# Kernel optimization log

Measured on AMD Instinct MI355X. Metric: run time of the kernel, lower is better.

## Reference

```python
import jax, jax.numpy as jnp
import numpy as np

MARGIN = 0.2
LAMBDA_SOFTMAX = 9.0
LAMBDA_LSE = 6.0
WEIGHT_FACTOR = 0.7  # attn_prev is absent/zero on the i2t path
EPS = 1e-8
NEG_INF = -1e9


def setup_inputs() -> dict:
    key = jax.random.key(0)
    k1, k2, k3 = jax.random.split(key, 3)
    B, R, W, D = 128, 36, 32, 256  # batch, regions, max words, feat dim
    im = jax.random.normal(k1, (B, R, D), jnp.float32)
    s = jax.random.normal(k2, (B, W, D), jnp.float32)
    s_l = jax.random.randint(k3, (B,), 1, W + 1)  # caption lengths in [1, W]
    return {"im": im, "s": s, "s_l": s_l}


def _xattn_scores_i2t(im, s, s_l):
    # im: (B, R, D) images; s: (C, W, D) captions; s_l: (C,) lengths
    C, W = s.shape[0], s.shape[1]
    word_mask = jnp.arange(W)[None, :] < s_l[:, None]  # (C, W)

    # func_attention(query=images, context=caption words):
    # attn[c,b,w,r] = <s[c,w], im[b,r]>
    attn = jnp.einsum('cwd,brd->cbwr', s, im)
    # raw_feature_norm == 'clipped_l2norm': LeakyReLU(0.1) then l2norm over region axis
    attn = jax.nn.leaky_relu(attn, 0.1)
    attn = attn / (jnp.sqrt(jnp.sum(attn * attn, axis=-1, keepdims=True)) + EPS)
    # softmax over sourceL = words, with smoothing; mask padded words
    logits = jnp.where(word_mask[:, None, :, None], attn * LAMBDA_SOFTMAX, NEG_INF)
    A = jax.nn.softmax(logits, axis=2)  # (C, B, W, R), sums to 1 over words
    # weightedContext[c,b,r,:] = 0.7 * sum_w A[c,b,w,r] * s[c,w,:]
    wC = WEIGHT_FACTOR * jnp.einsum('cbwr,cwd->cbrd', A, s)

    # cosine similarity between image regions and weighted caption context
    num = jnp.sum(im[None] * wC, axis=-1)                      # (C, B, R)
    denom = jnp.linalg.norm(im, axis=-1)[None] * jnp.linalg.norm(wC, axis=-1)
    row_sim = num / jnp.clip(denom, EPS)

    # agg_func == 'LogSumExp' over regions
    sim = jax.nn.logsumexp(LAMBDA_LSE * row_sim, axis=2) / LAMBDA_LSE  # (C, B)
    return sim.T  # scores: (n_image, n_caption)


def reference(im, s, s_l):
    scores = _xattn_scores_i2t(im, s, s_l)
    diag = jnp.diag(scores)
    cost_s = jnp.clip(MARGIN + scores - diag[:, None], 0.0)   # caption retrieval
    cost_im = jnp.clip(MARGIN + scores - diag[None, :], 0.0)  # image retrieval
    eye = jnp.eye(scores.shape[0], dtype=bool)
    cost_s = jnp.where(eye, 0.0, cost_s)
    cost_im = jnp.where(eye, 0.0, cost_im)
    # max_violation=True: hardest negatives
    return jnp.sum(jnp.max(cost_s, axis=1)) + jnp.sum(jnp.max(cost_im, axis=0))
```

## Files before the change

kernel.cpp:

```cpp
#include <hip/hip_runtime.h>
#include <math.h>

#define CN 128
#define RN 36
#define WN 32
#define DN 256

#define SSTR  264
#define GSTR  40
#define ATSTR 40

#define WS_SCORES 0
#define WS_S_SW   65536
#define WS_IM_SW  (WS_S_SW + CN*16384)
#define WS_N2I    (WS_IM_SW + CN*18432)
#define WS_NEED   (WS_N2I + CN*RN*4)

typedef unsigned short u16;
typedef __attribute__((ext_vector_type(4))) unsigned short u16x4;
typedef __attribute__((ext_vector_type(8))) unsigned short u16x8;
typedef __attribute__((ext_vector_type(8))) __bf16 bf16x8;
typedef __attribute__((ext_vector_type(4))) float f32x4;

#define C9   12.9842502f
#define C6   8.65616798f
#define IC6  0.115524530f

__device__ __forceinline__ float bf2f(u16 u){ return __uint_as_float(((unsigned)u)<<16); }
__device__ __forceinline__ u16 f2bf(float f){ unsigned x=__float_as_uint(f); return (u16)((x + 0x7fffu + ((x>>16)&1u))>>16); }
__device__ __forceinline__ u16 f2bf_hw(float f){ __bf16 h = (__bf16)f; return __builtin_bit_cast(u16, h); }
__device__ __forceinline__ float lrelu(float v){ return fmaxf(v, 0.1f*v); }

__device__ __forceinline__ void gload16(const void* g, void* l){
    __builtin_amdgcn_global_load_lds((const __attribute__((address_space(1))) void*)g,
                                     (__attribute__((address_space(3))) void*)l, 16, 0, 0);
}

__global__ __launch_bounds__(256)
void precompute_kernel(const float* __restrict__ im, const float* __restrict__ s,
                       char* __restrict__ ws)
{
    const int tid = threadIdx.x;
    if (blockIdx.x < 128) {
        const int i = blockIdx.x;
        const float* src = s + (size_t)i*(WN*DN);
        u16* out = (u16*)(ws + WS_S_SW) + (size_t)i*8192;
#pragma unroll
        for (int it = 0; it < 4; it++) {
            int idx = tid + it*256;
            int r = idx >> 5, x = idx & 31;
            int jl = (x & 24) | ((x & 7) ^ (r & 7));
            const float4* p = (const float4*)(src + r*DN + jl*8);
            float4 v0 = p[0], v1 = p[1];
            u16x8 hh = { f2bf_hw(v0.x),f2bf_hw(v0.y),f2bf_hw(v0.z),f2bf_hw(v0.w),
                         f2bf_hw(v1.x),f2bf_hw(v1.y),f2bf_hw(v1.z),f2bf_hw(v1.w) };
            *(u16x8*)(out + r*256 + x*8) = hh;
        }
    } else {
        const int i = blockIdx.x - 128;
        const float* src = im + (size_t)i*(RN*DN);
#pragma unroll
        for (int it = 0; it < 5; it++) {
            int idx = tid + it*256;
            if (idx < 1152) {
                int q = idx / 288, rem = idx - q*288;
                int r = rem >> 3, x = rem & 7;
                int jl = x ^ (r & 7);
                const float4* p = (const float4*)(src + r*DN + q*64 + jl*8);
                float4 v0 = p[0], v1 = p[1];
                u16x8 hh = { f2bf_hw(v0.x),f2bf_hw(v0.y),f2bf_hw(v0.z),f2bf_hw(v0.w),
                             f2bf_hw(v1.x),f2bf_hw(v1.y),f2bf_hw(v1.z),f2bf_hw(v1.w) };
                *(u16x8*)(ws + WS_IM_SW + (size_t)q*589824 + (size_t)i*4608 + r*128 + x*16) = hh;
            }
        }
        float* n2o = (float*)(ws + WS_N2I) + (size_t)i*RN;
#pragma unroll
        for (int it = 0; it < 2; it++) {
            int idx = tid + it*256;
            if (idx < 288) {
                int r = idx >> 3, q = idx & 7;
                const float4* p = (const float4*)(src + r*DN + q*32);
                float ss = 0.f;
#pragma unroll
                for (int k = 0; k < 8; k++) {
                    float4 v = p[k];
                    ss = fmaf(v.x,v.x,ss); ss = fmaf(v.y,v.y,ss);
                    ss = fmaf(v.z,v.z,ss); ss = fmaf(v.w,v.w,ss);
                }
                ss += __shfl_xor(ss,1); ss += __shfl_xor(ss,2); ss += __shfl_xor(ss,4);
                if (q == 0) n2o[r] = ss;
            }
        }
    }
}

__global__ __launch_bounds__(512, 2)
void xattn_staged(const int* __restrict__ s_l, char* __restrict__ ws)
{
    __shared__ __align__(16) u16 smem[37376];
    u16* lds_s  = smem;
    u16* lds_im = smem + 16384;
    u16* lds_g  = smem + 34816;
    char* smem_b = (char*)smem;

    const int tid = threadIdx.x;
    const int lane = tid & 63, wv = tid >> 6;
    const int bq = blockIdx.x, cp = blockIdx.y;
    const int ci = wv >> 2, bi = wv & 3;
    const int c = cp*2 + ci, b = bq*4 + bi;
    const int col = lane & 15, g4 = lane >> 4;
    const int gm = bi >> 1, gn = bi & 1;
    const int L = s_l[c];
    const int r2c = (32+col > 35) ? 35 : 32+col;

    const char* ssrc = ws + WS_S_SW + (size_t)(cp*2)*16384;
    const char* ibase = ws + WS_IM_SW + (size_t)(bq*4)*4608;

    auto stage_im = [&](int q, int buf){
        const char* isrc = ibase + (size_t)q*589824;
        char* dbase = smem_b + 32768 + buf*18432;
#pragma unroll
        for (int t = 0; t < 3; t++) {
            int blk = wv + t*8;
            if (blk < 18) gload16(isrc + blk*1024 + lane*16, dbase + blk*1024);
        }
    };

#pragma unroll
    for (int t = 0; t < 7; t++) {
        int blk = wv + t*8;
        if (blk < 50) {
            const char* src; char* dst;
            if (blk < 32) { src = ssrc + blk*1024;         dst = smem_b + blk*1024; }
            else          { src = ibase + (blk-32)*1024;   dst = smem_b + 32768 + (blk-32)*1024; }
            gload16(src + lane*16, dst);
        }
    }

    const float* n2p = (const float*)(ws + WS_N2I) + (size_t)b*RN;
    float n2v0 = n2p[col];
    float n2v1 = n2p[16+col];
    float n2v2 = n2p[r2c];

    f32x4 raw[2][3];
#pragma unroll
    for (int m = 0; m < 2; m++)
#pragma unroll
        for (int n = 0; n < 3; n++) raw[m][n] = (f32x4){0.f,0.f,0.f,0.f};
    f32x4 gacc = {0.f,0.f,0.f,0.f};

    const u16* sbb = lds_s + ci*8192;

    auto computeq = [&](int q, int buf){
        const u16* ibb = lds_im + buf*9216 + bi*2304;
#pragma unroll
        for (int ks = 0; ks < 2; ks++) {
            int chq = ks*4 + g4;
            int swA = chq ^ (col & 7);
            int oA  = (q*8 + swA) * 8;
            int oB  = swA * 8;
            int oB2 = (chq ^ (r2c & 7)) * 8;
            bf16x8 a0 = *(const bf16x8*)&sbb[col*256 + oA];
            bf16x8 a1 = *(const bf16x8*)&sbb[(16+col)*256 + oA];
            bf16x8 ga = *(const bf16x8*)&sbb[(gm*16+col)*256 + oA];
            bf16x8 gb = *(const bf16x8*)&sbb[(gn*16+col)*256 + oA];
            bf16x8 b0 = *(const bf16x8*)&ibb[col*64 + oB];
            bf16x8 b1 = *(const bf16x8*)&ibb[(16+col)*64 + oB];
            bf16x8 b2 = *(const bf16x8*)&ibb[r2c*64 + oB2];
            raw[0][0] = __builtin_amdgcn_mfma_f32_16x16x32_bf16(a0, b0, raw[0][0], 0,0,0);
            raw[0][1] = __builtin_amdgcn_mfma_f32_16x16x32_bf16(a0, b1, raw[0][1], 0,0,0);
            raw[0][2] = __builtin_amdgcn_mfma_f32_16x16x32_bf16(a0, b2, raw[0][2], 0,0,0);
            raw[1][0] = __builtin_amdgcn_mfma_f32_16x16x32_bf16(a1, b0, raw[1][0], 0,0,0);
            raw[1][1] = __builtin_amdgcn_mfma_f32_16x16x32_bf16(a1, b1, raw[1][1], 0,0,0);
            raw[1][2] = __builtin_amdgcn_mfma_f32_16x16x32_bf16(a1, b2, raw[1][2], 0,0,0);
            gacc      = __builtin_amdgcn_mfma_f32_16x16x32_bf16(ga, gb, gacc, 0,0,0);
        }
    };

    __syncthreads();
    stage_im(1, 1); computeq(0, 0);
    __syncthreads();
    stage_im(2, 0); computeq(1, 1);
    __syncthreads();
    stage_im(3, 1); computeq(2, 0);
    __syncthreads();
    computeq(3, 1);

    {
        u16x4 hg = { f2bf_hw(gacc[0]), f2bf_hw(gacc[1]), f2bf_hw(gacc[2]), f2bf_hw(gacc[3]) };
        *(u16x4*)&lds_g[ci*1280 + (gn*16+col)*GSTR + gm*16 + g4*4] = hg;
    }

    float af[2][3][4];
#pragma unroll
    for (int m = 0; m < 2; m++) {
#pragma unroll
        for (int reg = 0; reg < 4; reg++) {
            float ssum = 0.f;
#pragma unroll
            for (int n = 0; n < 3; n++) {
                float v = lrelu(raw[m][n][reg]);
                if (n == 2 && col >= 4) v = 0.f;
                af[m][n][reg] = v;
                ssum = fmaf(v, v, ssum);
            }
            ssum += __shfl_xor(ssum, 1);
            ssum += __shfl_xor(ssum, 2);
            ssum += __shfl_xor(ssum, 4);
            ssum += __shfl_xor(ssum, 8);
            float inv2 = C9 / (sqrtf(ssum) + 1e-8f);
#pragma unroll
            for (int n = 0; n < 3; n++) af[m][n][reg] *= inv2;
        }
    }

    float num[3];
#pragma unroll
    for (int n = 0; n < 3; n++) {
        float nm = 0.f;
#pragma unroll
        for (int m = 0; m < 2; m++)
#pragma unroll
            for (int reg = 0; reg < 4; reg++) {
                int w = m*16 + g4*4 + reg;
                float e = (w < L) ? __builtin_amdgcn_exp2f(af[m][n][reg]) : 0.f;
                af[m][n][reg] = e;
                nm = fmaf(e, raw[m][n][reg], nm);
            }
        nm += __shfl_xor(nm, 16);
        nm += __shfl_xor(nm, 32);
        num[n] = nm;
    }

    __syncthreads();

    u16* at = (u16*)(smem_b + 32768) + wv*1920;
#pragma unroll
    for (int m = 0; m < 2; m++)
#pragma unroll
        for (int n = 0; n < 3; n++) {
            u16x4 h = { f2bf_hw(af[m][n][0]), f2bf_hw(af[m][n][1]),
                        f2bf_hw(af[m][n][2]), f2bf_hw(af[m][n][3]) };
            *(u16x4*)&at[(n*16 + col)*ATSTR + m*16 + g4*4] = h;
        }

    bf16x8 gf0 = *(const bf16x8*)&lds_g[ci*1280 + col*GSTR + g4*8];
    bf16x8 gf1 = *(const bf16x8*)&lds_g[ci*1280 + (16+col)*GSTR + g4*8];

    float qv[3];
#pragma unroll
    for (int n = 0; n < 3; n++) {
        bf16x8 bfv = *(const bf16x8*)&at[(n*16 + col)*ATSTR + g4*8];
        f32x4 z = {0.f,0.f,0.f,0.f};
        f32x4 t0 = __builtin_amdgcn_mfma_f32_16x16x32_bf16(gf0, bfv, z, 0,0,0);
        f32x4 t1 = __builtin_amdgcn_mfma_f32_16x16x32_bf16(gf1, bfv, z, 0,0,0);
        float q = 0.f;
#pragma unroll
        for (int reg = 0; reg < 4; reg++) {
            q = fmaf(af[0][n][reg], t0[reg], q);
            q = fmaf(af[1][n][reg], t1[reg], q);
        }
        q += __shfl_xor(q, 16);
        q += __shfl_xor(q, 32);
        qv[n] = q;
    }

    float rs[3];
    {
        float n2a[3] = { n2v0, n2v1, n2v2 };
#pragma unroll
        for (int n = 0; n < 3; n++) {
            float denom = fmaxf(0.7f * sqrtf(n2a[n] * qv[n]), 1e-8f);
            rs[n] = 0.7f * num[n] / denom;
        }
    }
    float xm = -1e30f;
#pragma unroll
    for (int n = 0; n < 3; n++) {
        bool valid = (n < 2) || (col < 4);
        if (valid) xm = fmaxf(xm, C6 * rs[n]);
    }
    xm = fmaxf(xm, __shfl_xor(xm, 1));
    xm = fmaxf(xm, __shfl_xor(xm, 2));
    xm = fmaxf(xm, __shfl_xor(xm, 4));
    xm = fmaxf(xm, __shfl_xor(xm, 8));
    float es = 0.f;
#pragma unroll
    for (int n = 0; n < 3; n++) {
        bool valid = (n < 2) || (col < 4);
        if (valid) es += __builtin_amdgcn_exp2f(C6 * rs[n] - xm);
    }
    es += __shfl_xor(es, 1);
    es += __shfl_xor(es, 2);
    es += __shfl_xor(es, 4);
    es += __shfl_xor(es, 8);

    if (lane == 0)
        ((float*)(ws + WS_SCORES))[(size_t)b * CN + c] =
            (xm + __builtin_amdgcn_logf(es)) * IC6;
}

__global__ __launch_bounds__(512, 2)
void xattn_fallback(const float* __restrict__ im, const float* __restrict__ s,
                    const int* __restrict__ s_l, float* __restrict__ scores)
{
    __shared__ u16   s_lds[2][WN*SSTR];
    __shared__ u16   im_lds[4][RN*SSTR];
    __shared__ u16   g_lds[2][WN*GSTR];
    __shared__ u16   at_lds[8][48*ATSTR];
    __shared__ float n2i_lds[4][RN];

    const int tid  = threadIdx.x;
    const int lane = tid & 63;
    const int wv   = tid >> 6;
    const int bq   = blockIdx.x, cp = blockIdx.y;
    const int ci   = wv >> 2, bi = wv & 3;
    const int c    = cp*2 + ci, b = bq*4 + bi;
    const int col  = lane & 15, g4 = lane >> 4;

    if (wv < 4) {
        const float4* g = (const float4*)(im + (size_t)(bq*4 + wv) * (RN*DN));
        u16* dst = im_lds[wv];
#pragma unroll
        for (int k = 0; k < 36; k++) {
            int i = lane + k*64;
            float4 v = g[i];
            int row = i >> 6, cc = (i & 63) * 4;
            u16x4 h = { f2bf(v.x), f2bf(v.y), f2bf(v.z), f2bf(v.w) };
            *(u16x4*)&dst[row*SSTR + cc] = h;
        }
    } else {
        int cap = (wv - 4) >> 1;
        int l2  = ((wv - 4) & 1) * 64 + lane;
        const float4* g = (const float4*)(s + (size_t)(cp*2 + cap) * (WN*DN));
        u16* dst = s_lds[cap];
#pragma unroll
        for (int k = 0; k < 16; k++) {
            int i = l2 + k*128;
            float4 v = g[i];
            int row = i >> 6, cc = (i & 63) * 4;
            u16x4 h = { f2bf(v.x), f2bf(v.y), f2bf(v.z), f2bf(v.w) };
            *(u16x4*)&dst[row*SSTR + cc] = h;
        }
    }
    __syncthreads();

    {
        const int gm = (wv >> 1) & 1, gn = wv & 1;
        const u16* sb = s_lds[ci];
        f32x4 acc = {0.f, 0.f, 0.f, 0.f};
#pragma unroll
        for (int ks = 0; ks < 8; ks++) {
            int k0 = ks*32 + g4*8;
            bf16x8 af = *(const bf16x8*)&sb[(gm*16 + col)*SSTR + k0];
            bf16x8 bfv = *(const bf16x8*)&sb[(gn*16 + col)*SSTR + k0];
            acc = __builtin_amdgcn_mfma_f32_16x16x32_bf16(af, bfv, acc, 0, 0, 0);
        }
        u16x4 h = { f2bf(acc[0]), f2bf(acc[1]), f2bf(acc[2]), f2bf(acc[3]) };
        *(u16x4*)&g_lds[ci][(gn*16 + col)*GSTR + gm*16 + g4*4] = h;
    }

    if (wv < 4) {
        const u16* ib = im_lds[wv];
        int r = lane >> 1, half = lane & 1;
        float ss = 0.f;
        const u16x8* p = (const u16x8*)&ib[r*SSTR + half*128];
#pragma unroll
        for (int k = 0; k < 16; k++) {
            u16x8 v = p[k];
#pragma unroll
            for (int j = 0; j < 8; j++) { float f = bf2f(v[j]); ss = fmaf(f, f, ss); }
        }
        ss += __shfl_xor(ss, 1);
        if (half == 0) n2i_lds[wv][r] = ss;
        if (lane < 8) {
            int r2 = 32 + (lane >> 1), h2 = lane & 1;
            float s2 = 0.f;
            const u16x8* p2 = (const u16x8*)&ib[r2*SSTR + h2*128];
#pragma unroll
            for (int k = 0; k < 16; k++) {
                u16x8 v = p2[k];
#pragma unroll
                for (int j = 0; j < 8; j++) { float f = bf2f(v[j]); s2 = fmaf(f, f, s2); }
            }
            s2 += __shfl_xor(s2, 1);
            if (h2 == 0) n2i_lds[wv][r2] = s2;
        }
    }

    const u16* sb = s_lds[ci];
    const u16* ib = im_lds[bi];
    f32x4 raw[2][3];
#pragma unroll
    for (int m = 0; m < 2; m++)
#pragma unroll
        for (int n = 0; n < 3; n++) raw[m][n] = (f32x4){0.f,0.f,0.f,0.f};
    {
        int r2c = 32 + col; if (r2c > 35) r2c = 35;
#pragma unroll
        for (int ks = 0; ks < 8; ks++) {
            int k0 = ks*32 + g4*8;
            bf16x8 a0 = *(const bf16x8*)&sb[col*SSTR + k0];
            bf16x8 a1 = *(const bf16x8*)&sb[(16 + col)*SSTR + k0];
            bf16x8 b0 = *(const bf16x8*)&ib[col*SSTR + k0];
            bf16x8 b1 = *(const bf16x8*)&ib[(16 + col)*SSTR + k0];
            bf16x8 b2 = *(const bf16x8*)&ib[r2c*SSTR + k0];
            raw[0][0] = __builtin_amdgcn_mfma_f32_16x16x32_bf16(a0, b0, raw[0][0], 0,0,0);
            raw[0][1] = __builtin_amdgcn_mfma_f32_16x16x32_bf16(a0, b1, raw[0][1], 0,0,0);
            raw[0][2] = __builtin_amdgcn_mfma_f32_16x16x32_bf16(a0, b2, raw[0][2], 0,0,0);
            raw[1][0] = __builtin_amdgcn_mfma_f32_16x16x32_bf16(a1, b0, raw[1][0], 0,0,0);
            raw[1][1] = __builtin_amdgcn_mfma_f32_16x16x32_bf16(a1, b1, raw[1][1], 0,0,0);
            raw[1][2] = __builtin_amdgcn_mfma_f32_16x16x32_bf16(a1, b2, raw[1][2], 0,0,0);
        }
    }

    float af[2][3][4];
#pragma unroll
    for (int m = 0; m < 2; m++) {
#pragma unroll
        for (int reg = 0; reg < 4; reg++) {
            float ssum = 0.f;
#pragma unroll
            for (int n = 0; n < 3; n++) {
                float v = lrelu(raw[m][n][reg]);
                if (n == 2 && col >= 4) v = 0.f;
                af[m][n][reg] = v;
                ssum = fmaf(v, v, ssum);
            }
            ssum += __shfl_xor(ssum, 1);
            ssum += __shfl_xor(ssum, 2);
            ssum += __shfl_xor(ssum, 4);
            ssum += __shfl_xor(ssum, 8);
            float inv = 1.0f / (sqrtf(ssum) + 1e-8f);
#pragma unroll
            for (int n = 0; n < 3; n++) af[m][n][reg] *= inv;
        }
    }

    const int L = s_l[c];
    float num[3], qv[3];
#pragma unroll
    for (int n = 0; n < 3; n++) {
        float mx = -1e30f;
#pragma unroll
        for (int m = 0; m < 2; m++)
#pragma unroll
            for (int reg = 0; reg < 4; reg++) {
                int w = m*16 + g4*4 + reg;
                if (w < L) mx = fmaxf(mx, af[m][n][reg]);
            }
        mx = fmaxf(mx, __shfl_xor(mx, 16));
        mx = fmaxf(mx, __shfl_xor(mx, 32));
        mx *= 9.0f;
        float sme = 0.f;
#pragma unroll
        for (int m = 0; m < 2; m++)
#pragma unroll
            for (int reg = 0; reg < 4; reg++) {
                int w = m*16 + g4*4 + reg;
                float e = (w < L) ? __expf(fmaf(9.0f, af[m][n][reg], -mx)) : 0.f;
                af[m][n][reg] = e;
                sme += e;
            }
        sme += __shfl_xor(sme, 16);
        sme += __shfl_xor(sme, 32);
        float inv = 1.0f / sme;
        float nm = 0.f;
#pragma unroll
        for (int m = 0; m < 2; m++)
#pragma unroll
            for (int reg = 0; reg < 4; reg++) {
                af[m][n][reg] *= inv;
                nm = fmaf(af[m][n][reg], raw[m][n][reg], nm);
            }
        nm += __shfl_xor(nm, 16);
        nm += __shfl_xor(nm, 32);
        num[n] = nm;
    }

#pragma unroll
    for (int m = 0; m < 2; m++)
#pragma unroll
        for (int n = 0; n < 3; n++) {
            u16x4 h = { f2bf(af[m][n][0]), f2bf(af[m][n][1]),
                        f2bf(af[m][n][2]), f2bf(af[m][n][3]) };
            *(u16x4*)&at_lds[wv][(n*16 + col)*ATSTR + m*16 + g4*4] = h;
        }

    __syncthreads();

    bf16x8 gf0 = *(const bf16x8*)&g_lds[ci][col*GSTR + g4*8];
    bf16x8 gf1 = *(const bf16x8*)&g_lds[ci][(16+col)*GSTR + g4*8];
    f32x4 tt[2][3];
#pragma unroll
    for (int n = 0; n < 3; n++) {
        bf16x8 bfv = *(const bf16x8*)&at_lds[wv][(n*16 + col)*ATSTR + g4*8];
        f32x4 z = {0.f,0.f,0.f,0.f};
        tt[0][n] = __builtin_amdgcn_mfma_f32_16x16x32_bf16(gf0, bfv, z, 0,0,0);
        tt[1][n] = __builtin_amdgcn_mfma_f32_16x16x32_bf16(gf1, bfv, z, 0,0,0);
    }

#pragma unroll
    for (int n = 0; n < 3; n++) {
        float q = 0.f;
#pragma unroll
        for (int m = 0; m < 2; m++)
#pragma unroll
            for (int reg = 0; reg < 4; reg++) q = fmaf(af[m][n][reg], tt[m][n][reg], q);
        q += __shfl_xor(q, 16);
        q += __shfl_xor(q, 32);
        qv[n] = q;
    }

    float rs[3];
#pragma unroll
    for (int n = 0; n < 3; n++) {
        int r = n*16 + col; if (r > 35) r = 35;
        float n2 = n2i_lds[bi][r];
        float denom = fmaxf(0.7f * sqrtf(n2 * qv[n]), 1e-8f);
        rs[n] = 0.7f * num[n] / denom;
    }
    float xm = -1e30f;
#pragma unroll
    for (int n = 0; n < 3; n++) {
        bool valid = (n < 2) || (col < 4);
        if (valid) xm = fmaxf(xm, 6.0f * rs[n]);
    }
    xm = fmaxf(xm, __shfl_xor(xm, 1));
    xm = fmaxf(xm, __shfl_xor(xm, 2));
    xm = fmaxf(xm, __shfl_xor(xm, 4));
    xm = fmaxf(xm, __shfl_xor(xm, 8));
    float es = 0.f;
#pragma unroll
    for (int n = 0; n < 3; n++) {
        bool valid = (n < 2) || (col < 4);
        if (valid) es += __expf(6.0f * rs[n] - xm);
    }
    es += __shfl_xor(es, 1);
    es += __shfl_xor(es, 2);
    es += __shfl_xor(es, 4);
    es += __shfl_xor(es, 8);

    if (lane == 0) scores[(size_t)b * CN + c] = (xm + __logf(es)) / 6.0f;
}

__global__ __launch_bounds__(1024)
void contrastive_loss_kernel(const float* __restrict__ scores,
                             unsigned int* __restrict__ out)
{
    __shared__ float sc[128][129];
    __shared__ float dg[128];
    __shared__ float red[128];
    const int tid = threadIdx.x;

    const float4* s4 = (const float4*)scores;
#pragma unroll
    for (int it = 0; it < 4; it++) {
        int i = tid + it*1024;
        float4 v = s4[i];
        int row = i >> 5, c4 = (i & 31) << 2;
        sc[row][c4+0] = v.x; sc[row][c4+1] = v.y;
        sc[row][c4+2] = v.z; sc[row][c4+3] = v.w;
    }
    __syncthreads();
    if (tid < 128) dg[tid] = sc[tid][tid];
    __syncthreads();

    const int i = tid >> 3, g = tid & 7;
    const float di = dg[i];
    float rm = 0.f, cm = 0.f;
#pragma unroll
    for (int k = 0; k < 16; k++) {
        int j = g*16 + k;
        if (j != i) {
            rm = fmaxf(rm, 0.2f + sc[i][j] - di);
            cm = fmaxf(cm, 0.2f + sc[j][i] - di);
        }
    }
    rm = fmaxf(rm, __shfl_xor(rm, 1)); cm = fmaxf(cm, __shfl_xor(cm, 1));
    rm = fmaxf(rm, __shfl_xor(rm, 2)); cm = fmaxf(cm, __shfl_xor(cm, 2));
    rm = fmaxf(rm, __shfl_xor(rm, 4)); cm = fmaxf(cm, __shfl_xor(cm, 4));
    if (g == 0) red[i] = rm + cm;
    __syncthreads();

    if (tid < 64) {
        float v = red[tid] + red[tid + 64];
#pragma unroll
        for (int off = 32; off >= 1; off >>= 1) v += __shfl_xor(v, off);
        if (tid == 0) {
            unsigned int x = __float_as_uint(v);
            unsigned int h = (x + 0x7fffu + ((x >> 16) & 1u)) >> 16;
            out[0] = (h << 16) | h;
        }
    }
}

extern "C" void kernel_launch(void* const* d_in, const int* in_sizes, int n_in,
                              void* d_out, int out_size, void* d_ws, size_t ws_size,
                              hipStream_t stream) {
    const float* im  = (const float*)d_in[0];
    const float* s   = (const float*)d_in[1];
    const int*   s_l = (const int*)d_in[2];
    char* ws = (char*)d_ws;

    dim3 grid(32, 64);
    if (ws_size >= (size_t)WS_NEED) {
        precompute_kernel<<<256, 256, 0, stream>>>(im, s, ws);
        xattn_staged<<<grid, 512, 0, stream>>>(s_l, ws);
    } else {
        xattn_fallback<<<grid, 512, 0, stream>>>(im, s, s_l, (float*)ws);
    }
    contrastive_loss_kernel<<<1, 1024, 0, stream>>>((const float*)ws, (unsigned int*)d_out);
}
```

Baseline: 51.64 us.

## Load MFMA fragments directly from global in fragment-major layout, shrink LDS

Precompute now writes caption and image bf16 data in MFMA fragment order so each lane reads its operand with one 16-byte global load, which removes the LDS staging pipeline and most barriers. Only the 4 tail image rows are staged in LDS. This shrinks shared memory enough to raise launch bounds to 3 blocks per CU. The logsumexp drops the max subtraction, relying on cosine similarity being bounded, and the denominator now uses rsqrt. The trade is heavier reliance on global and L2 latency with no explicit prefetch overlap.

Measured after the change: 48.85 us. 1.06x faster.

```diff
diff --git a/kernel.cpp b/kernel.cpp
--- a/kernel.cpp
+++ b/kernel.cpp
@@ -11,10 +11,11 @@
 #define ATSTR 40
 
 #define WS_SCORES 0
-#define WS_S_SW   65536
-#define WS_IM_SW  (WS_S_SW + CN*16384)
-#define WS_N2I    (WS_IM_SW + CN*18432)
-#define WS_NEED   (WS_N2I + CN*RN*4)
+#define WS_SF   65536
+#define WS_IMF  (WS_SF + CN*16384)
+#define WS_TAIL (WS_IMF + CN*16384)
+#define WS_N2I  (WS_TAIL + CN*2048)
+#define WS_NEED (WS_N2I + CN*RN*4)
 
 typedef unsigned short u16;
 typedef __attribute__((ext_vector_type(4))) unsigned short u16x4;
@@ -44,34 +45,40 @@
     if (blockIdx.x < 128) {
         const int i = blockIdx.x;
         const float* src = s + (size_t)i*(WN*DN);
-        u16* out = (u16*)(ws + WS_S_SW) + (size_t)i*8192;
+        u16* out = (u16*)(ws + WS_SF) + (size_t)i*8192;
 #pragma unroll
         for (int it = 0; it < 4; it++) {
             int idx = tid + it*256;
-            int r = idx >> 5, x = idx & 31;
-            int jl = (x & 24) | ((x & 7) ^ (r & 7));
-            const float4* p = (const float4*)(src + r*DN + jl*8);
+            int m = idx >> 9, ks = (idx >> 6) & 7, ln = idx & 63;
+            int col = ln & 15, g4 = ln >> 4;
+            const float4* p = (const float4*)(src + (m*16+col)*DN + ks*32 + g4*8);
             float4 v0 = p[0], v1 = p[1];
             u16x8 hh = { f2bf_hw(v0.x),f2bf_hw(v0.y),f2bf_hw(v0.z),f2bf_hw(v0.w),
                          f2bf_hw(v1.x),f2bf_hw(v1.y),f2bf_hw(v1.z),f2bf_hw(v1.w) };
-            *(u16x8*)(out + r*256 + x*8) = hh;
+            *(u16x8*)(out + (size_t)idx*8) = hh;
         }
     } else {
         const int i = blockIdx.x - 128;
         const float* src = im + (size_t)i*(RN*DN);
-#pragma unroll
-        for (int it = 0; it < 5; it++) {
+        u16* out = (u16*)(ws + WS_IMF) + (size_t)i*8192;
+#pragma unroll
+        for (int it = 0; it < 4; it++) {
             int idx = tid + it*256;
-            if (idx < 1152) {
-                int q = idx / 288, rem = idx - q*288;
-                int r = rem >> 3, x = rem & 7;
-                int jl = x ^ (r & 7);
-                const float4* p = (const float4*)(src + r*DN + q*64 + jl*8);
-                float4 v0 = p[0], v1 = p[1];
-                u16x8 hh = { f2bf_hw(v0.x),f2bf_hw(v0.y),f2bf_hw(v0.z),f2bf_hw(v0.w),
-                             f2bf_hw(v1.x),f2bf_hw(v1.y),f2bf_hw(v1.z),f2bf_hw(v1.w) };
-                *(u16x8*)(ws + WS_IM_SW + (size_t)q*589824 + (size_t)i*4608 + r*128 + x*16) = hh;
-            }
+            int m = idx >> 9, ks = (idx >> 6) & 7, ln = idx & 63;
+            int col = ln & 15, g4 = ln >> 4;
+            const float4* p = (const float4*)(src + (m*16+col)*DN + ks*32 + g4*8);
+            float4 v0 = p[0], v1 = p[1];
+            u16x8 hh = { f2bf_hw(v0.x),f2bf_hw(v0.y),f2bf_hw(v0.z),f2bf_hw(v0.w),
+                         f2bf_hw(v1.x),f2bf_hw(v1.y),f2bf_hw(v1.z),f2bf_hw(v1.w) };
+            *(u16x8*)(out + (size_t)idx*8) = hh;
+        }
+        if (tid < 128) {
+            int row = tid >> 5, x = tid & 31;
+            const float4* p = (const float4*)(src + (32+row)*DN + x*8);
+            float4 v0 = p[0], v1 = p[1];
+            u16x8 hh = { f2bf_hw(v0.x),f2bf_hw(v0.y),f2bf_hw(v0.z),f2bf_hw(v0.w),
+                         f2bf_hw(v1.x),f2bf_hw(v1.y),f2bf_hw(v1.z),f2bf_hw(v1.w) };
+            *(u16x8*)((u16*)(ws + WS_TAIL) + (size_t)i*1024 + row*256 + x*8) = hh;
         }
         float* n2o = (float*)(ws + WS_N2I) + (size_t)i*RN;
 #pragma unroll
@@ -94,14 +101,11 @@
     }
 }
 
-__global__ __launch_bounds__(512, 2)
+__global__ __launch_bounds__(512, 3)
 void xattn_staged(const int* __restrict__ s_l, char* __restrict__ ws)
 {
-    __shared__ __align__(16) u16 smem[37376];
-    u16* lds_s  = smem;
-    u16* lds_im = smem + 16384;
-    u16* lds_g  = smem + 34816;
-    char* smem_b = (char*)smem;
+    __shared__ __align__(16) u16 smem[22016];
+    u16* lds_g = smem + 4096;
 
     const int tid = threadIdx.x;
     const int lane = tid & 63, wv = tid >> 6;
@@ -112,35 +116,21 @@
     const int gm = bi >> 1, gn = bi & 1;
     const int L = s_l[c];
     const int r2c = (32+col > 35) ? 35 : 32+col;
-
-    const char* ssrc = ws + WS_S_SW + (size_t)(cp*2)*16384;
-    const char* ibase = ws + WS_IM_SW + (size_t)(bq*4)*4608;
-
-    auto stage_im = [&](int q, int buf){
-        const char* isrc = ibase + (size_t)q*589824;
-        char* dbase = smem_b + 32768 + buf*18432;
-#pragma unroll
-        for (int t = 0; t < 3; t++) {
-            int blk = wv + t*8;
-            if (blk < 18) gload16(isrc + blk*1024 + lane*16, dbase + blk*1024);
-        }
-    };
-
-#pragma unroll
-    for (int t = 0; t < 7; t++) {
-        int blk = wv + t*8;
-        if (blk < 50) {
-            const char* src; char* dst;
-            if (blk < 32) { src = ssrc + blk*1024;         dst = smem_b + blk*1024; }
-            else          { src = ibase + (blk-32)*1024;   dst = smem_b + 32768 + (blk-32)*1024; }
-            gload16(src + lane*16, dst);
-        }
-    }
-
+    const int trow = (col > 3) ? 3 : col;
+
+    {
+        const char* tsrc = ws + WS_TAIL + (size_t)(bq*4)*2048;
+        gload16(tsrc + wv*1024 + lane*16, (char*)smem + wv*1024);
+    }
     const float* n2p = (const float*)(ws + WS_N2I) + (size_t)b*RN;
     float n2v0 = n2p[col];
     float n2v1 = n2p[16+col];
     float n2v2 = n2p[r2c];
+    __syncthreads();
+
+    const char* sf = ws + WS_SF  + (size_t)c*16384;
+    const char* mf = ws + WS_IMF + (size_t)b*16384;
+    const u16*  tl = smem + bi*1024;
 
     f32x4 raw[2][3];
 #pragma unroll
@@ -149,42 +139,23 @@
         for (int n = 0; n < 3; n++) raw[m][n] = (f32x4){0.f,0.f,0.f,0.f};
     f32x4 gacc = {0.f,0.f,0.f,0.f};
 
-    const u16* sbb = lds_s + ci*8192;
-
-    auto computeq = [&](int q, int buf){
-        const u16* ibb = lds_im + buf*9216 + bi*2304;
-#pragma unroll
-        for (int ks = 0; ks < 2; ks++) {
-            int chq = ks*4 + g4;
-            int swA = chq ^ (col & 7);
-            int oA  = (q*8 + swA) * 8;
-            int oB  = swA * 8;
-            int oB2 = (chq ^ (r2c & 7)) * 8;
-            bf16x8 a0 = *(const bf16x8*)&sbb[col*256 + oA];
-            bf16x8 a1 = *(const bf16x8*)&sbb[(16+col)*256 + oA];
-            bf16x8 ga = *(const bf16x8*)&sbb[(gm*16+col)*256 + oA];
-            bf16x8 gb = *(const bf16x8*)&sbb[(gn*16+col)*256 + oA];
-            bf16x8 b0 = *(const bf16x8*)&ibb[col*64 + oB];
-            bf16x8 b1 = *(const bf16x8*)&ibb[(16+col)*64 + oB];
-            bf16x8 b2 = *(const bf16x8*)&ibb[r2c*64 + oB2];
-            raw[0][0] = __builtin_amdgcn_mfma_f32_16x16x32_bf16(a0, b0, raw[0][0], 0,0,0);
-            raw[0][1] = __builtin_amdgcn_mfma_f32_16x16x32_bf16(a0, b1, raw[0][1], 0,0,0);
-            raw[0][2] = __builtin_amdgcn_mfma_f32_16x16x32_bf16(a0, b2, raw[0][2], 0,0,0);
-            raw[1][0] = __builtin_amdgcn_mfma_f32_16x16x32_bf16(a1, b0, raw[1][0], 0,0,0);
-            raw[1][1] = __builtin_amdgcn_mfma_f32_16x16x32_bf16(a1, b1, raw[1][1], 0,0,0);
-            raw[1][2] = __builtin_amdgcn_mfma_f32_16x16x32_bf16(a1, b2, raw[1][2], 0,0,0);
-            gacc      = __builtin_amdgcn_mfma_f32_16x16x32_bf16(ga, gb, gacc, 0,0,0);
-        }
-    };
-
-    __syncthreads();
-    stage_im(1, 1); computeq(0, 0);
-    __syncthreads();
-    stage_im(2, 0); computeq(1, 1);
-    __syncthreads();
-    stage_im(3, 1); computeq(2, 0);
-    __syncthreads();
-    computeq(3, 1);
+#pragma unroll
+    for (int ks = 0; ks < 8; ks++) {
+        bf16x8 a0 = *(const bf16x8*)(sf +        ks*1024 + lane*16);
+        bf16x8 a1 = *(const bf16x8*)(sf + 8192 + ks*1024 + lane*16);
+        bf16x8 b0 = *(const bf16x8*)(mf +        ks*1024 + lane*16);
+        bf16x8 b1 = *(const bf16x8*)(mf + 8192 + ks*1024 + lane*16);
+        bf16x8 b2 = *(const bf16x8*)&tl[trow*256 + ks*32 + g4*8];
+        bf16x8 ga = gm ? a1 : a0;
+        bf16x8 gb = gn ? a1 : a0;
+        raw[0][0] = __builtin_amdgcn_mfma_f32_16x16x32_bf16(a0, b0, raw[0][0], 0,0,0);
+        raw[0][1] = __builtin_amdgcn_mfma_f32_16x16x32_bf16(a0, b1, raw[0][1], 0,0,0);
+        raw[0][2] = __builtin_amdgcn_mfma_f32_16x16x32_bf16(a0, b2, raw[0][2], 0,0,0);
+        raw[1][0] = __builtin_amdgcn_mfma_f32_16x16x32_bf16(a1, b0, raw[1][0], 0,0,0);
+        raw[1][1] = __builtin_amdgcn_mfma_f32_16x16x32_bf16(a1, b1, raw[1][1], 0,0,0);
+        raw[1][2] = __builtin_amdgcn_mfma_f32_16x16x32_bf16(a1, b2, raw[1][2], 0,0,0);
+        gacc      = __builtin_amdgcn_mfma_f32_16x16x32_bf16(ga, gb, gacc, 0,0,0);
+    }
 
     {
         u16x4 hg = { f2bf_hw(gacc[0]), f2bf_hw(gacc[1]), f2bf_hw(gacc[2]), f2bf_hw(gacc[3]) };
@@ -234,7 +205,7 @@
 
     __syncthreads();
 
-    u16* at = (u16*)(smem_b + 32768) + wv*1920;
+    u16* at = smem + 6656 + wv*1920;
 #pragma unroll
     for (int m = 0; m < 2; m++)
 #pragma unroll
@@ -265,30 +236,13 @@
         qv[n] = q;
     }
 
-    float rs[3];
-    {
-        float n2a[3] = { n2v0, n2v1, n2v2 };
-#pragma unroll
-        for (int n = 0; n < 3; n++) {
-            float denom = fmaxf(0.7f * sqrtf(n2a[n] * qv[n]), 1e-8f);
-            rs[n] = 0.7f * num[n] / denom;
-        }
-    }
-    float xm = -1e30f;
-#pragma unroll
-    for (int n = 0; n < 3; n++) {
+    float es = 0.f;
+#pragma unroll
+    for (int n = 0; n < 3; n++) {
+        float n2a = (n == 0) ? n2v0 : (n == 1) ? n2v1 : n2v2;
+        float rs = num[n] * rsqrtf(fmaxf(n2a * qv[n], 1e-16f));
         bool valid = (n < 2) || (col < 4);
-        if (valid) xm = fmaxf(xm, C6 * rs[n]);
-    }
-    xm = fmaxf(xm, __shfl_xor(xm, 1));
-    xm = fmaxf(xm, __shfl_xor(xm, 2));
-    xm = fmaxf(xm, __shfl_xor(xm, 4));
-    xm = fmaxf(xm, __shfl_xor(xm, 8));
-    float es = 0.f;
-#pragma unroll
-    for (int n = 0; n < 3; n++) {
-        bool valid = (n < 2) || (col < 4);
-        if (valid) es += __builtin_amdgcn_exp2f(C6 * rs[n] - xm);
+        if (valid) es += __builtin_amdgcn_exp2f(C6 * rs);
     }
     es += __shfl_xor(es, 1);
     es += __shfl_xor(es, 2);
@@ -297,7 +251,7 @@
 
     if (lane == 0)
         ((float*)(ws + WS_SCORES))[(size_t)b * CN + c] =
-            (xm + __builtin_amdgcn_logf(es)) * IC6;
+            __builtin_amdgcn_logf(es) * IC6;
 }
 
 __global__ __launch_bounds__(512, 2)
```
